# Kernel optimization log

Hardware: AMD Instinct MI355X
Metric: run time of the kernel (lower is better)

## Reference

```python
import jax, jax.numpy as jnp
import numpy as np

V, E, H, B, T, O = 100000, 300, 512, 512, 64, 2


def setup_inputs() -> dict:
    key = jax.random.key(0)
    ks = jax.random.split(key, 12)
    bound = 1.0 / np.sqrt(H)
    u = lambda k, shape: jax.random.uniform(k, shape, jnp.float32, -bound, bound)
    tokens = jax.random.randint(ks[0], (B, T), 0, V)  # int token ids
    emb = jax.random.normal(ks[1], (V, E), jnp.float32) * 0.05  # pretrained embeddings
    # GRU params stacked over 2 directions: [2, 3H, in], [2, 3H, H], [2, 3H]
    w_ih0 = u(ks[2], (2, 3 * H, E))
    w_hh0 = u(ks[3], (2, 3 * H, H))
    b_ih0 = u(ks[4], (2, 3 * H))
    b_hh0 = u(ks[5], (2, 3 * H))
    w_ih1 = u(ks[6], (2, 3 * H, 2 * H))
    w_hh1 = u(ks[7], (2, 3 * H, H))
    b_ih1 = u(ks[8], (2, 3 * H))
    b_hh1 = u(ks[9], (2, 3 * H))
    fc_w = u(ks[10], (O, 2 * H))
    fc_b = u(ks[11], (O,))
    return dict(tokens=tokens, emb=emb, w_ih0=w_ih0, w_hh0=w_hh0, b_ih0=b_ih0,
                b_hh0=b_hh0, w_ih1=w_ih1, w_hh1=w_hh1, b_ih1=b_ih1, b_hh1=b_hh1,
                fc_w=fc_w, fc_b=fc_b)


def _gru_dir(x, Wih, Whh, bih, bhh):
    # x: [B, T, in] -> [B, T, H]; PyTorch GRU cell math.
    gx = jnp.einsum('bti,gi->btg', x, Wih) + bih  # input gates precomputed [B,T,3H]
    h_units = Whh.shape[1]

    def step(h, g):
        gh = h @ Whh.T + bhh
        xr, xz, xn = jnp.split(g, 3, axis=-1)
        hr, hz, hn = jnp.split(gh, 3, axis=-1)
        r = jax.nn.sigmoid(xr + hr)
        z = jax.nn.sigmoid(xz + hz)
        n = jnp.tanh(xn + r * hn)
        h_new = (1.0 - z) * n + z * h
        return h_new, h_new

    h0 = jnp.zeros((x.shape[0], h_units), x.dtype)
    _, ys = jax.lax.scan(step, h0, jnp.swapaxes(gx, 0, 1))  # scan over time
    return jnp.swapaxes(ys, 0, 1)


def _gru_bidir(x, w_ih, w_hh, b_ih, b_hh):
    fwd = _gru_dir(x, w_ih[0], w_hh[0], b_ih[0], b_hh[0])
    bwd = _gru_dir(x[:, ::-1], w_ih[1], w_hh[1], b_ih[1], b_hh[1])[:, ::-1]
    return jnp.concatenate([fwd, bwd], axis=-1)  # [B, T, 2H]


def reference(tokens, emb, w_ih0, w_hh0, b_ih0, b_hh0, w_ih1, w_hh1, b_ih1,
              b_hh1, fc_w, fc_b):
    x = emb[tokens]                                   # [B, T, E]
    h1 = _gru_bidir(x, w_ih0, w_hh0, b_ih0, b_hh0)    # [B, T, 2H]
    h2 = _gru_bidir(h1, w_ih1, w_hh1, b_ih1, b_hh1)   # [B, T, 2H]
    # dropout output is discarded in the original forward (out = output[:, -1, :])
    last = h2[:, -1, :]                               # [B, 2H]
    return last @ fc_w.T + fc_b                       # [B, O]
```

## Files before the change

kernel.cpp:

```cpp
#include <hip/hip_runtime.h>
#include <stdint.h>


#define NTW 192
#define MTX 2048

typedef _Float16 half8 __attribute__((ext_vector_type(8)));
typedef _Float16 half4_t __attribute__((ext_vector_type(4)));
typedef float float4_t __attribute__((ext_vector_type(4)));

__device__ __forceinline__ void gl_lds16(const void* g, void* l) {
  __builtin_amdgcn_global_load_lds(
      (const __attribute__((address_space(1))) void*)g,
      (__attribute__((address_space(3))) void*)l, 16, 0, 0);
}

__device__ __forceinline__ float sigm_f(float x) { return 1.f / (1.f + __expf(-x)); }
__device__ __forceinline__ float tanh_f(float x) { return 1.f - 2.f / (__expf(2.f * x) + 1.f); }

__global__ void pack_b_kernel(const float* __restrict__ src, _Float16* __restrict__ dst,
                              int K, int KI) {
  int gid = blockIdx.x * 256 + threadIdx.x;
  int l = gid & 63, unit = gid >> 6;
  int nt = unit / KI, ks = unit - nt * KI;
  if (nt >= NTW) return;
  int row = nt * 16 + (l & 15);
  int col0 = ks * 32 + ((l >> 4) << 3);
  half8 v;
#pragma unroll
  for (int j = 0; j < 8; ++j) {
    int c = col0 + j;
    v[j] = (c < K) ? (_Float16)src[(long)row * K + c] : (_Float16)0.f;
  }
  *(half8*)(dst + (long)unit * 512 + l * 8) = v;
}

__global__ void gather_kernel(const int* __restrict__ tokens, const float* __restrict__ emb,
                              _Float16* __restrict__ x0) {
  int gid = blockIdx.x * 256 + threadIdx.x;
  int l = gid & 63, unit = gid >> 6;
  int mt = unit / 10, ks = unit - mt * 10;
  if (mt >= MTX) return;
  int row = mt * 16 + (l & 15);
  const float* e = emb + (long)tokens[row] * 300;
  int col0 = ks * 32 + ((l >> 4) << 3);
  half8 v;
#pragma unroll
  for (int j = 0; j < 8; ++j) {
    int c = col0 + j;
    v[j] = (c < 300) ? (_Float16)e[c] : (_Float16)0.f;
  }
  *(half8*)(x0 + (long)unit * 512 + l * 8) = v;
}

__global__ __launch_bounds__(256) void gemm_bt_kernel(
    const _Float16* __restrict__ A, const _Float16* __restrict__ Bw,
    const float* __restrict__ bias, _Float16* __restrict__ C, int KI) {
  __shared__ _Float16 As[8 * 512];
  __shared__ _Float16 Bs[8 * 512];
  const int bx = blockIdx.x, by = blockIdx.y;
  const int tid = threadIdx.x, w = tid >> 6, l = tid & 63;
  const int wm = w >> 1, wn = w & 1, ln = l & 15;
  const int mt0 = by * 8, nt0 = bx * 8;
  float4_t acc[4][4];
#pragma unroll
  for (int i = 0; i < 4; ++i)
#pragma unroll
    for (int j = 0; j < 4; ++j) acc[i][j] = 0.f;
  for (int it = 0; it < KI; ++it) {
    __syncthreads();
    gl_lds16(A + ((long)(mt0 + w) * KI + it) * 512 + l * 8, As + w * 512 + l * 8);
    gl_lds16(A + ((long)(mt0 + w + 4) * KI + it) * 512 + l * 8, As + (w + 4) * 512 + l * 8);
    gl_lds16(Bw + ((long)(nt0 + w) * KI + it) * 512 + l * 8, Bs + w * 512 + l * 8);
    gl_lds16(Bw + ((long)(nt0 + w + 4) * KI + it) * 512 + l * 8, Bs + (w + 4) * 512 + l * 8);
    __syncthreads();
    half8 af[4], bf[4];
#pragma unroll
    for (int i = 0; i < 4; ++i) af[i] = *(const half8*)(As + (wm * 4 + i) * 512 + l * 8);
#pragma unroll
    for (int j = 0; j < 4; ++j) bf[j] = *(const half8*)(Bs + (wn * 4 + j) * 512 + l * 8);
#pragma unroll
    for (int i = 0; i < 4; ++i)
#pragma unroll
      for (int j = 0; j < 4; ++j)
        acc[i][j] = __builtin_amdgcn_mfma_f32_16x16x32_f16(af[i], bf[j], acc[i][j], 0, 0, 0);
  }
#pragma unroll
  for (int i = 0; i < 4; ++i)
#pragma unroll
    for (int j = 0; j < 4; ++j) {
      int mt = mt0 + wm * 4 + i, ntile = nt0 + wn * 4 + j;
      float bv = bias[ntile * 16 + ln];
      half4_t o;
#pragma unroll
      for (int r = 0; r < 4; ++r) o[r] = (_Float16)(acc[i][j][r] + bv);
      *(half4_t*)(C + ((long)mt * NTW + ntile) * 256 + l * 4) = o;
    }
}

__global__ __launch_bounds__(256, 1) void gru_scan_kernel(
    const _Float16* __restrict__ whh,
    const float* __restrict__ bhh,
    const _Float16* __restrict__ gx,
    _Float16* hbuf, _Float16* ys,
    float* last,
    unsigned int* cnt) {
  __shared__ alignas(16) _Float16 hx[4 * 512];
  const int bid = blockIdx.x;
  const int d = bid >> 7, mtb = (bid >> 4) & 7, nt = bid & 15;
  const int tid = threadIdx.x, w = tid >> 6, l = tid & 63;
  const int wm = w >> 1, wn = w & 1, lq = l >> 4, ln = l & 15;
  unsigned int* flags = cnt + (d * 8 + mtb) * 16;
  const int hcol = nt * 32 + wn * 16 + ln;

  half8 bf[3][16];
#pragma unroll
  for (int g = 0; g < 3; ++g) {
    const int tg = d * 96 + g * 32 + nt * 2 + wn;
#pragma unroll
    for (int ks = 0; ks < 16; ++ks)
      bf[g][ks] = *(const half8*)(whh + (long)(tg * 16 + ks) * 512 + l * 8);
  }
  const float bh0 = bhh[d * 1536 + hcol];
  const float bh1 = bhh[d * 1536 + 512 + hcol];
  const float bh2 = bhh[d * 1536 + 1024 + hcol];
  float hreg[2][4] = {{0.f, 0.f, 0.f, 0.f}, {0.f, 0.f, 0.f, 0.f}};
  const int mtr0 = mtb * 4 + wm * 2;
  const int qh = (hcol >> 3) & 3, jh = hcol & 7;
  const int ntg0 = d * 96 + nt * 2 + wn;
  const unsigned long long* hb8 = (const unsigned long long*)hbuf;

  float xr[2][4], xz[2][4], xn[2][4];
  auto load_gx = [&](int step, float (&vr)[2][4], float (&vz)[2][4], float (&vn)[2][4]) {
    const int t2 = d ? (63 - step) : step;
    const int rm2 = t2 & 15, tq2 = t2 >> 4;
    const int eoff2 = ((rm2 >> 2) * 16 + ln) * 4 + (rm2 & 3);
#pragma unroll
    for (int i = 0; i < 2; ++i)
#pragma unroll
      for (int r = 0; r < 4; ++r) {
        const int b = (mtr0 + i) * 16 + lq * 4 + r;
        const long gbase = ((long)(b * 4 + tq2) * 192 + ntg0) * 256 + eoff2;
        vr[i][r] = (float)gx[gbase];
        vz[i][r] = (float)gx[gbase + 32 * 256];
        vn[i][r] = (float)gx[gbase + 64 * 256];
      }
  };
  load_gx(0, xr, xz, xn);

  for (int s = 0; s < 64; ++s) {
    const int par = s & 1;
    const unsigned long long* hr8 = hb8 + (long)(d * 2 + par) * 65536;
    const int t_in = d ? (63 - s) : s;
    const int rm = t_in & 15, tq = t_in >> 4;

    float4_t acc[3][2];
#pragma unroll
    for (int g = 0; g < 3; ++g) { acc[g][0] = 0.f; acc[g][1] = 0.f; }
#pragma unroll
    for (int kk = 0; kk < 2; ++kk) {
      half8 af[2][8];
#pragma unroll
      for (int i = 0; i < 2; ++i)
#pragma unroll
        for (int k2 = 0; k2 < 8; ++k2) {
          const unsigned long long* p =
              hr8 + ((long)(mtr0 + i) * 16 + kk * 8 + k2) * 128 + l * 2;
          union { half8 h; unsigned long long q[2]; } fu;
          fu.q[0] = __hip_atomic_load(p, __ATOMIC_RELAXED, __HIP_MEMORY_SCOPE_AGENT);
          fu.q[1] = __hip_atomic_load(p + 1, __ATOMIC_RELAXED, __HIP_MEMORY_SCOPE_AGENT);
          af[i][k2] = fu.h;
        }
#pragma unroll
      for (int k2 = 0; k2 < 8; ++k2)
#pragma unroll
        for (int i = 0; i < 2; ++i)
#pragma unroll
          for (int g = 0; g < 3; ++g)
            acc[g][i] = __builtin_amdgcn_mfma_f32_16x16x32_f16(af[i][k2], bf[g][kk * 8 + k2],
                                                               acc[g][i], 0, 0, 0);
    }

#pragma unroll
    for (int i = 0; i < 2; ++i) {
      const int mtile_i = mtr0 + i;
#pragma unroll
      for (int r = 0; r < 4; ++r) {
        const int b = mtile_i * 16 + lq * 4 + r;
        const long gmt = (long)b * 4 + tq;
        const float rg = sigm_f(xr[i][r] + acc[0][i][r] + bh0);
        const float zg = sigm_f(xz[i][r] + acc[1][i][r] + bh1);
        const float ng = tanh_f(xn[i][r] + rg * (acc[2][i][r] + bh2));
        const float hv = (1.f - zg) * ng + zg * hreg[i][r];
        hreg[i][r] = hv;
        hx[(wm * 2 + i) * 512 + (qh * 16 + lq * 4 + r) * 8 + jh] = (_Float16)hv;
        if (ys != nullptr) {
          const int kcol = d * 512 + hcol;
          ys[(gmt * 32 + (kcol >> 5)) * 512 + (((kcol >> 3) & 3) * 16 + rm) * 8 + (kcol & 7)] =
              (_Float16)hv;
        }
        if (last != nullptr && ((d == 0 && s == 63) || (d == 1 && s == 0)))
          last[(long)b * 1024 + d * 512 + hcol] = hv;
      }
    }
    if (s == 63) break;

    __syncthreads();
    {
      const int u = tid >> 6, lw = tid & 63;
      union { half8 h; unsigned long long q[2]; } wb;
      wb.h = *(const half8*)(hx + u * 512 + lw * 8);
      unsigned long long* dst = (unsigned long long*)hbuf +
                                (long)(d * 2 + (par ^ 1)) * 65536 +
                                ((long)((mtb * 4 + u) * 16 + nt)) * 128 + lw * 2;
      __hip_atomic_store(dst, wb.q[0], __ATOMIC_RELAXED, __HIP_MEMORY_SCOPE_AGENT);
      __hip_atomic_store(dst + 1, wb.q[1], __ATOMIC_RELAXED, __HIP_MEMORY_SCOPE_AGENT);
    }
    __syncthreads();

    if (tid == 0)
      __hip_atomic_store(flags + nt, (unsigned int)(s + 1), __ATOMIC_RELAXED,
                         __HIP_MEMORY_SCOPE_AGENT);

    load_gx(s + 1, xr, xz, xn);

    {
      const unsigned int tgt = (unsigned int)(s + 1);
      long guard = 0;
      for (;;) {
        const unsigned int f = __hip_atomic_load(flags + (l & 15), __ATOMIC_RELAXED,
                                                 __HIP_MEMORY_SCOPE_AGENT);
        if (__all((int)(f >= tgt))) break;
        __builtin_amdgcn_s_sleep(1);
        if (++guard > (1L << 24)) break;
      }
      __builtin_amdgcn_fence(__ATOMIC_ACQUIRE, "workgroup");
    }
  }
}

__global__ void fc_kernel(const float* __restrict__ lastb, const float* __restrict__ fw,
                          const float* __restrict__ fb, float* __restrict__ out) {
  const int b = blockIdx.x, l = threadIdx.x;
  const float* x = lastb + (long)b * 1024;
  float a0 = 0.f, a1 = 0.f;
  for (int k = l; k < 1024; k += 64) {
    const float v = x[k];
    a0 += v * fw[k];
    a1 += v * fw[1024 + k];
  }
#pragma unroll
  for (int off = 32; off > 0; off >>= 1) {
    a0 += __shfl_down(a0, off, 64);
    a1 += __shfl_down(a1, off, 64);
  }
  if (l == 0) {
    out[b * 2 + 0] = a0 + fb[0];
    out[b * 2 + 1] = a1 + fb[1];
  }
}

extern "C" void kernel_launch(void* const* d_in, const int* in_sizes, int n_in,
                              void* d_out, int out_size, void* d_ws, size_t ws_size,
                              hipStream_t stream) {
  const int* tokens = (const int*)d_in[0];
  const float* emb = (const float*)d_in[1];
  const float* w_ih0 = (const float*)d_in[2];
  const float* w_hh0 = (const float*)d_in[3];
  const float* b_ih0 = (const float*)d_in[4];
  const float* b_hh0 = (const float*)d_in[5];
  const float* w_ih1 = (const float*)d_in[6];
  const float* w_hh1 = (const float*)d_in[7];
  const float* b_ih1 = (const float*)d_in[8];
  const float* b_hh1 = (const float*)d_in[9];
  const float* fc_w = (const float*)d_in[10];
  const float* fc_b = (const float*)d_in[11];
  float* out = (float*)d_out;

  char* ws = (char*)d_ws;
  size_t off = 0;
  auto alloc = [&](size_t bytes) -> void* {
    void* p = ws + off;
    off += (bytes + 255) & ~(size_t)255;
    return p;
  };
  _Float16* W0f = (_Float16*)alloc(192L * 10 * 512 * 2);
  _Float16* W1f = (_Float16*)alloc(192L * 32 * 512 * 2);
  _Float16* Wh0f = (_Float16*)alloc(192L * 16 * 512 * 2);
  _Float16* Wh1f = (_Float16*)alloc(192L * 16 * 512 * 2);
  _Float16* x0f = (_Float16*)alloc(2048L * 10 * 512 * 2);
  _Float16* x1f = (_Float16*)alloc(2048L * 32 * 512 * 2);
  _Float16* gxb = (_Float16*)alloc(2048L * 192 * 256 * 2);
  char* hz = ws + off;
  _Float16* hbuf = (_Float16*)alloc(4L * 32 * 8192 * 2);
  unsigned int* cnt = (unsigned int*)alloc(4096);
  const size_t hz_bytes = 4L * 32 * 8192 * 2 + 4096;
  float* lastb = (float*)alloc(512L * 1024 * 4);
  if (off > ws_size) return;

  pack_b_kernel<<<dim3(192 * 10 * 64 / 256), 256, 0, stream>>>(w_ih0, W0f, 300, 10);
  pack_b_kernel<<<dim3(192 * 32 * 64 / 256), 256, 0, stream>>>(w_ih1, W1f, 1024, 32);
  pack_b_kernel<<<dim3(192 * 16 * 64 / 256), 256, 0, stream>>>(w_hh0, Wh0f, 512, 16);
  pack_b_kernel<<<dim3(192 * 16 * 64 / 256), 256, 0, stream>>>(w_hh1, Wh1f, 512, 16);
  gather_kernel<<<dim3(2048 * 10 * 64 / 256), 256, 0, stream>>>(tokens, emb, x0f);

  gemm_bt_kernel<<<dim3(24, 256), 256, 0, stream>>>(x0f, W0f, b_ih0, gxb, 10);
  hipMemsetAsync(hz, 0, hz_bytes, stream);
  gru_scan_kernel<<<dim3(256), 256, 0, stream>>>(Wh0f, b_hh0, gxb, hbuf, x1f, nullptr, cnt);

  gemm_bt_kernel<<<dim3(24, 256), 256, 0, stream>>>(x1f, W1f, b_ih1, gxb, 32);
  hipMemsetAsync(hz, 0, hz_bytes, stream);
  gru_scan_kernel<<<dim3(256), 256, 0, stream>>>(Wh1f, b_hh1, gxb, hbuf, nullptr, lastb, cnt);

  fc_kernel<<<dim3(512), 64, 0, stream>>>(lastb, fc_w, fc_b, out);
}
```

Before: 1.437 ms.

## Regroup scan blocks by batch rows and stage hidden state through LDS

Changes the block decomposition of the recurrent scan: each block now owns 2 M-tiles (32 batch rows) and 64 hidden columns instead of 4 M-tiles and 32 columns. Each sync group therefore shrinks from 16 to 8 blocks. Each step, the block cooperatively copies the shared hidden state once into a 32 KB LDS buffer, and all warps read it from there, replacing per-warp redundant atomic global loads. This cuts global traffic per step and lowers the barrier fan-in. The cost is an extra LDS round trip and __syncthreads per step, plus higher LDS use.

```diff
diff --git a/kernel.cpp b/kernel.cpp
--- a/kernel.cpp
+++ b/kernel.cpp
@@ -105,18 +105,19 @@
     _Float16* hbuf, _Float16* ys,
     float* last,
     unsigned int* cnt) {
+  __shared__ alignas(16) _Float16 hs[32 * 512];
   __shared__ alignas(16) _Float16 hx[4 * 512];
   const int bid = blockIdx.x;
-  const int d = bid >> 7, mtb = (bid >> 4) & 7, nt = bid & 15;
+  const int d = bid >> 7, mtg = (bid >> 3) & 15, ntb = bid & 7;
   const int tid = threadIdx.x, w = tid >> 6, l = tid & 63;
-  const int wm = w >> 1, wn = w & 1, lq = l >> 4, ln = l & 15;
-  unsigned int* flags = cnt + (d * 8 + mtb) * 16;
-  const int hcol = nt * 32 + wn * 16 + ln;
+  const int lq = l >> 4, ln = l & 15;
+  unsigned int* flags = cnt + (d * 16 + mtg) * 16;
+  const int hcol = ntb * 64 + w * 16 + ln;
 
   half8 bf[3][16];
 #pragma unroll
   for (int g = 0; g < 3; ++g) {
-    const int tg = d * 96 + g * 32 + nt * 2 + wn;
+    const int tg = d * 96 + g * 32 + ntb * 4 + w;
 #pragma unroll
     for (int ks = 0; ks < 16; ++ks)
       bf[g][ks] = *(const half8*)(whh + (long)(tg * 16 + ks) * 512 + l * 8);
@@ -125,10 +126,10 @@
   const float bh1 = bhh[d * 1536 + 512 + hcol];
   const float bh2 = bhh[d * 1536 + 1024 + hcol];
   float hreg[2][4] = {{0.f, 0.f, 0.f, 0.f}, {0.f, 0.f, 0.f, 0.f}};
-  const int mtr0 = mtb * 4 + wm * 2;
-  const int qh = (hcol >> 3) & 3, jh = hcol & 7;
-  const int ntg0 = d * 96 + nt * 2 + wn;
+  const int mtr0 = mtg * 2;
+  const int ntg0 = d * 96 + ntb * 4 + w;
   const unsigned long long* hb8 = (const unsigned long long*)hbuf;
+  unsigned long long* lds64 = (unsigned long long*)hs;
 
   float xr[2][4], xz[2][4], xn[2][4];
   auto load_gx = [&](int step, float (&vr)[2][4], float (&vz)[2][4], float (&vn)[2][4]) {
@@ -150,10 +151,33 @@
 
   for (int s = 0; s < 64; ++s) {
     const int par = s & 1;
-    const unsigned long long* hr8 = hb8 + (long)(d * 2 + par) * 65536;
     const int t_in = d ? (63 - s) : s;
     const int rm = t_in & 15, tq = t_in >> 4;
 
+    {
+      const unsigned long long* src =
+          hb8 + (long)(d * 2 + par) * 65536 + (long)mtg * 4096;
+#pragma unroll
+      for (int rr = 0; rr < 2; ++rr) {
+        unsigned long long t0[8];
+#pragma unroll
+        for (int j = 0; j < 4; ++j) {
+          const int f = (rr * 4 + j) * 256 + tid;
+          t0[j * 2] = __hip_atomic_load(src + (long)f * 2, __ATOMIC_RELAXED,
+                                        __HIP_MEMORY_SCOPE_AGENT);
+          t0[j * 2 + 1] = __hip_atomic_load(src + (long)f * 2 + 1, __ATOMIC_RELAXED,
+                                            __HIP_MEMORY_SCOPE_AGENT);
+        }
+#pragma unroll
+        for (int j = 0; j < 4; ++j) {
+          const int f = (rr * 4 + j) * 256 + tid;
+          lds64[f * 2] = t0[j * 2];
+          lds64[f * 2 + 1] = t0[j * 2 + 1];
+        }
+      }
+    }
+    __syncthreads();
+
     float4_t acc[3][2];
 #pragma unroll
     for (int g = 0; g < 3; ++g) { acc[g][0] = 0.f; acc[g][1] = 0.f; }
@@ -163,14 +187,8 @@
 #pragma unroll
       for (int i = 0; i < 2; ++i)
 #pragma unroll
-        for (int k2 = 0; k2 < 8; ++k2) {
-          const unsigned long long* p =
-              hr8 + ((long)(mtr0 + i) * 16 + kk * 8 + k2) * 128 + l * 2;
-          union { half8 h; unsigned long long q[2]; } fu;
-          fu.q[0] = __hip_atomic_load(p, __ATOMIC_RELAXED, __HIP_MEMORY_SCOPE_AGENT);
-          fu.q[1] = __hip_atomic_load(p + 1, __ATOMIC_RELAXED, __HIP_MEMORY_SCOPE_AGENT);
-          af[i][k2] = fu.h;
-        }
+        for (int k2 = 0; k2 < 8; ++k2)
+          af[i][k2] = *(const half8*)(hs + (i * 16 + kk * 8 + k2) * 512 + l * 8);
 #pragma unroll
       for (int k2 = 0; k2 < 8; ++k2)
 #pragma unroll
@@ -193,7 +211,8 @@
         const float ng = tanh_f(xn[i][r] + rg * (acc[2][i][r] + bh2));
         const float hv = (1.f - zg) * ng + zg * hreg[i][r];
         hreg[i][r] = hv;
-        hx[(wm * 2 + i) * 512 + (qh * 16 + lq * 4 + r) * 8 + jh] = (_Float16)hv;
+        hx[(i * 2 + (w >> 1)) * 512 + (((w & 1) * 2 + (ln >> 3)) * 16 + lq * 4 + r) * 8 +
+           (ln & 7)] = (_Float16)hv;
         if (ys != nullptr) {
           const int kcol = d * 512 + hcol;
           ys[(gmt * 32 + (kcol >> 5)) * 512 + (((kcol >> 3) & 3) * 16 + rm) * 8 + (kcol & 7)] =
@@ -212,14 +231,15 @@
       wb.h = *(const half8*)(hx + u * 512 + lw * 8);
       unsigned long long* dst = (unsigned long long*)hbuf +
                                 (long)(d * 2 + (par ^ 1)) * 65536 +
-                                ((long)((mtb * 4 + u) * 16 + nt)) * 128 + lw * 2;
+                                ((long)((mtg * 2 + (u >> 1)) * 16 + ntb * 2 + (u & 1))) * 128 +
+                                lw * 2;
       __hip_atomic_store(dst, wb.q[0], __ATOMIC_RELAXED, __HIP_MEMORY_SCOPE_AGENT);
       __hip_atomic_store(dst + 1, wb.q[1], __ATOMIC_RELAXED, __HIP_MEMORY_SCOPE_AGENT);
     }
     __syncthreads();
 
     if (tid == 0)
-      __hip_atomic_store(flags + nt, (unsigned int)(s + 1), __ATOMIC_RELAXED,
+      __hip_atomic_store(flags + ntb, (unsigned int)(s + 1), __ATOMIC_RELAXED,
                          __HIP_MEMORY_SCOPE_AGENT);
 
     load_gx(s + 1, xr, xz, xn);
@@ -228,7 +248,7 @@
       const unsigned int tgt = (unsigned int)(s + 1);
       long guard = 0;
       for (;;) {
-        const unsigned int f = __hip_atomic_load(flags + (l & 15), __ATOMIC_RELAXED,
+        const unsigned int f = __hip_atomic_load(flags + (l & 7), __ATOMIC_RELAXED,
                                                  __HIP_MEMORY_SCOPE_AGENT);
         if (__all((int)(f >= tgt))) break;
         __builtin_amdgcn_s_sleep(1);
```

New measurement: 1.264 ms. -12.0%, faster.

## Split GRU scan across 512 blocks with LDS-staged hidden state and streamed n-gate weights

Applied to the files above, without the earlier changes.

The persistent GRU scan now launches 512 workgroups instead of 256 (two per CU via launch bounds). Each block owns one 16-row batch tile and 64 hidden columns, and synchronises only with the 8 blocks sharing its batch tile. The hidden state is bulk-loaded into LDS once per step rather than each wave doing its own atomic global loads. To fit the register budget for two blocks per CU, only the r and z weights stay in registers and the n-gate weights are reloaded from global memory each step. The polling moves to the start of the step, so that weight reload overlaps the wait. This trades more per-step weight traffic and more blocks to coordinate for higher occupancy and a smaller working set per block.

```diff
diff --git a/kernel.cpp b/kernel.cpp
--- a/kernel.cpp
+++ b/kernel.cpp
@@ -98,144 +98,163 @@
     }
 }
 
-__global__ __launch_bounds__(256, 1) void gru_scan_kernel(
+__global__ __launch_bounds__(256, 2) void gru_scan_kernel(
     const _Float16* __restrict__ whh,
     const float* __restrict__ bhh,
     const _Float16* __restrict__ gx,
     _Float16* hbuf, _Float16* ys,
     float* last,
     unsigned int* cnt) {
-  __shared__ alignas(16) _Float16 hx[4 * 512];
+  __shared__ alignas(16) _Float16 hs[16 * 512];
+  __shared__ alignas(16) _Float16 hx[2 * 512];
   const int bid = blockIdx.x;
-  const int d = bid >> 7, mtb = (bid >> 4) & 7, nt = bid & 15;
+  const int d = bid >> 8, rt = (bid >> 3) & 31, ntb = bid & 7;
   const int tid = threadIdx.x, w = tid >> 6, l = tid & 63;
-  const int wm = w >> 1, wn = w & 1, lq = l >> 4, ln = l & 15;
-  unsigned int* flags = cnt + (d * 8 + mtb) * 16;
-  const int hcol = nt * 32 + wn * 16 + ln;
-
-  half8 bf[3][16];
-#pragma unroll
-  for (int g = 0; g < 3; ++g) {
-    const int tg = d * 96 + g * 32 + nt * 2 + wn;
-#pragma unroll
-    for (int ks = 0; ks < 16; ++ks)
-      bf[g][ks] = *(const half8*)(whh + (long)(tg * 16 + ks) * 512 + l * 8);
+  const int lq = l >> 4, ln = l & 15;
+  unsigned int* flags = cnt + (d * 32 + rt) * 16;
+  const int hcol = ntb * 64 + w * 16 + ln;
+
+  const int tgr = d * 96 + ntb * 4 + w;
+  const int tgz = tgr + 32;
+  const int tgn = tgr + 64;
+  half8 bfr[16], bfz[16];
+#pragma unroll
+  for (int ks = 0; ks < 16; ++ks) {
+    bfr[ks] = *(const half8*)(whh + (long)(tgr * 16 + ks) * 512 + l * 8);
+    bfz[ks] = *(const half8*)(whh + (long)(tgz * 16 + ks) * 512 + l * 8);
   }
   const float bh0 = bhh[d * 1536 + hcol];
   const float bh1 = bhh[d * 1536 + 512 + hcol];
   const float bh2 = bhh[d * 1536 + 1024 + hcol];
-  float hreg[2][4] = {{0.f, 0.f, 0.f, 0.f}, {0.f, 0.f, 0.f, 0.f}};
-  const int mtr0 = mtb * 4 + wm * 2;
-  const int qh = (hcol >> 3) & 3, jh = hcol & 7;
-  const int ntg0 = d * 96 + nt * 2 + wn;
+  float hreg[4] = {0.f, 0.f, 0.f, 0.f};
+  const int ntg0 = d * 96 + ntb * 4 + w;
   const unsigned long long* hb8 = (const unsigned long long*)hbuf;
-
-  float xr[2][4], xz[2][4], xn[2][4];
-  auto load_gx = [&](int step, float (&vr)[2][4], float (&vz)[2][4], float (&vn)[2][4]) {
+  unsigned long long* hb8w = (unsigned long long*)hbuf;
+  unsigned long long* lds64 = (unsigned long long*)hs;
+  const unsigned long long* hx64 = (const unsigned long long*)hx;
+
+  float xr[4], xz[4], xn[4];
+  auto load_gx = [&](int step) {
     const int t2 = d ? (63 - step) : step;
     const int rm2 = t2 & 15, tq2 = t2 >> 4;
     const int eoff2 = ((rm2 >> 2) * 16 + ln) * 4 + (rm2 & 3);
 #pragma unroll
-    for (int i = 0; i < 2; ++i)
-#pragma unroll
-      for (int r = 0; r < 4; ++r) {
-        const int b = (mtr0 + i) * 16 + lq * 4 + r;
-        const long gbase = ((long)(b * 4 + tq2) * 192 + ntg0) * 256 + eoff2;
-        vr[i][r] = (float)gx[gbase];
-        vz[i][r] = (float)gx[gbase + 32 * 256];
-        vn[i][r] = (float)gx[gbase + 64 * 256];
-      }
+    for (int r = 0; r < 4; ++r) {
+      const int b = rt * 16 + lq * 4 + r;
+      const long gbase = ((long)(b * 4 + tq2) * 192 + ntg0) * 256 + eoff2;
+      xr[r] = (float)gx[gbase];
+      xz[r] = (float)gx[gbase + 32 * 256];
+      xn[r] = (float)gx[gbase + 64 * 256];
+    }
   };
-  load_gx(0, xr, xz, xn);
+  load_gx(0);
+
+  auto poll = [&](unsigned int tgt) {
+    long guard = 0;
+    for (;;) {
+      const unsigned int f = __hip_atomic_load(flags + (l & 7), __ATOMIC_RELAXED,
+                                               __HIP_MEMORY_SCOPE_AGENT);
+      if (__all((int)(f >= tgt))) break;
+      __builtin_amdgcn_s_sleep(1);
+      if (++guard > (1L << 24)) break;
+    }
+  };
 
   for (int s = 0; s < 64; ++s) {
     const int par = s & 1;
-    const unsigned long long* hr8 = hb8 + (long)(d * 2 + par) * 65536;
     const int t_in = d ? (63 - s) : s;
     const int rm = t_in & 15, tq = t_in >> 4;
-
-    float4_t acc[3][2];
-#pragma unroll
-    for (int g = 0; g < 3; ++g) { acc[g][0] = 0.f; acc[g][1] = 0.f; }
-#pragma unroll
-    for (int kk = 0; kk < 2; ++kk) {
-      half8 af[2][8];
-#pragma unroll
-      for (int i = 0; i < 2; ++i)
-#pragma unroll
-        for (int k2 = 0; k2 < 8; ++k2) {
-          const unsigned long long* p =
-              hr8 + ((long)(mtr0 + i) * 16 + kk * 8 + k2) * 128 + l * 2;
-          union { half8 h; unsigned long long q[2]; } fu;
-          fu.q[0] = __hip_atomic_load(p, __ATOMIC_RELAXED, __HIP_MEMORY_SCOPE_AGENT);
-          fu.q[1] = __hip_atomic_load(p + 1, __ATOMIC_RELAXED, __HIP_MEMORY_SCOPE_AGENT);
-          af[i][k2] = fu.h;
-        }
-#pragma unroll
-      for (int k2 = 0; k2 < 8; ++k2)
-#pragma unroll
-        for (int i = 0; i < 2; ++i)
-#pragma unroll
-          for (int g = 0; g < 3; ++g)
-            acc[g][i] = __builtin_amdgcn_mfma_f32_16x16x32_f16(af[i][k2], bf[g][kk * 8 + k2],
-                                                               acc[g][i], 0, 0, 0);
-    }
-
-#pragma unroll
-    for (int i = 0; i < 2; ++i) {
-      const int mtile_i = mtr0 + i;
-#pragma unroll
-      for (int r = 0; r < 4; ++r) {
-        const int b = mtile_i * 16 + lq * 4 + r;
-        const long gmt = (long)b * 4 + tq;
-        const float rg = sigm_f(xr[i][r] + acc[0][i][r] + bh0);
-        const float zg = sigm_f(xz[i][r] + acc[1][i][r] + bh1);
-        const float ng = tanh_f(xn[i][r] + rg * (acc[2][i][r] + bh2));
-        const float hv = (1.f - zg) * ng + zg * hreg[i][r];
-        hreg[i][r] = hv;
-        hx[(wm * 2 + i) * 512 + (qh * 16 + lq * 4 + r) * 8 + jh] = (_Float16)hv;
-        if (ys != nullptr) {
-          const int kcol = d * 512 + hcol;
-          ys[(gmt * 32 + (kcol >> 5)) * 512 + (((kcol >> 3) & 3) * 16 + rm) * 8 + (kcol & 7)] =
-              (_Float16)hv;
-        }
-        if (last != nullptr && ((d == 0 && s == 63) || (d == 1 && s == 0)))
-          last[(long)b * 1024 + d * 512 + hcol] = hv;
+    const unsigned long long* src =
+        hb8 + (long)(d * 2 + par) * 65536 + (long)rt * 2048;
+
+    half8 bn0[8];
+#pragma unroll
+    for (int k = 0; k < 8; ++k)
+      bn0[k] = *(const half8*)(whh + (long)(tgn * 16 + k) * 512 + l * 8);
+
+    poll((unsigned int)s);
+    __builtin_amdgcn_fence(__ATOMIC_ACQUIRE, "workgroup");
+
+    unsigned long long ta[8];
+#pragma unroll
+    for (int j = 0; j < 8; ++j)
+      ta[j] = __hip_atomic_load(src + j * 256 + tid, __ATOMIC_RELAXED,
+                                __HIP_MEMORY_SCOPE_AGENT);
+#pragma unroll
+    for (int j = 0; j < 8; ++j) lds64[j * 256 + tid] = ta[j];
+    __syncthreads();
+
+    half8 bn1[8];
+#pragma unroll
+    for (int k = 0; k < 8; ++k)
+      bn1[k] = *(const half8*)(whh + (long)(tgn * 16 + 8 + k) * 512 + l * 8);
+
+    float4_t accr, accz, accn;
+    accr = 0.f; accz = 0.f; accn = 0.f;
+#pragma unroll
+    for (int c = 0; c < 2; ++c) {
+      half8 af[4];
+#pragma unroll
+      for (int k = 0; k < 4; ++k)
+        af[k] = *(const half8*)(hs + (c * 4 + k) * 512 + l * 8);
+#pragma unroll
+      for (int k = 0; k < 4; ++k) {
+        const int ks = c * 4 + k;
+        accr = __builtin_amdgcn_mfma_f32_16x16x32_f16(af[k], bfr[ks], accr, 0, 0, 0);
+        accz = __builtin_amdgcn_mfma_f32_16x16x32_f16(af[k], bfz[ks], accz, 0, 0, 0);
+        accn = __builtin_amdgcn_mfma_f32_16x16x32_f16(af[k], bn0[ks], accn, 0, 0, 0);
       }
     }
+#pragma unroll
+    for (int c = 0; c < 2; ++c) {
+      half8 af[4];
+#pragma unroll
+      for (int k = 0; k < 4; ++k)
+        af[k] = *(const half8*)(hs + ((8 + c * 4 + k)) * 512 + l * 8);
+#pragma unroll
+      for (int k = 0; k < 4; ++k) {
+        const int ks = 8 + c * 4 + k;
+        accr = __builtin_amdgcn_mfma_f32_16x16x32_f16(af[k], bfr[ks], accr, 0, 0, 0);
+        accz = __builtin_amdgcn_mfma_f32_16x16x32_f16(af[k], bfz[ks], accz, 0, 0, 0);
+        accn = __builtin_amdgcn_mfma_f32_16x16x32_f16(af[k], bn1[c * 4 + k], accn, 0, 0, 0);
+      }
+    }
+
+#pragma unroll
+    for (int r = 0; r < 4; ++r) {
+      const int b = rt * 16 + lq * 4 + r;
+      const long gmt = (long)b * 4 + tq;
+      const float rg = sigm_f(xr[r] + accr[r] + bh0);
+      const float zg = sigm_f(xz[r] + accz[r] + bh1);
+      const float ng = tanh_f(xn[r] + rg * (accn[r] + bh2));
+      const float hv = (1.f - zg) * ng + zg * hreg[r];
+      hreg[r] = hv;
+      hx[(w >> 1) * 512 + (((w & 1) * 2 + (ln >> 3)) * 16 + lq * 4 + r) * 8 + (ln & 7)] =
+          (_Float16)hv;
+      if (ys != nullptr) {
+        const int kcol = d * 512 + hcol;
+        ys[(gmt * 32 + (kcol >> 5)) * 512 + (((kcol >> 3) & 3) * 16 + rm) * 8 + (kcol & 7)] =
+            (_Float16)hv;
+      }
+      if (last != nullptr && ((d == 0 && s == 63) || (d == 1 && s == 0)))
+        last[(long)b * 1024 + d * 512 + hcol] = hv;
+    }
     if (s == 63) break;
 
     __syncthreads();
     {
-      const int u = tid >> 6, lw = tid & 63;
-      union { half8 h; unsigned long long q[2]; } wb;
-      wb.h = *(const half8*)(hx + u * 512 + lw * 8);
-      unsigned long long* dst = (unsigned long long*)hbuf +
-                                (long)(d * 2 + (par ^ 1)) * 65536 +
-                                ((long)((mtb * 4 + u) * 16 + nt)) * 128 + lw * 2;
-      __hip_atomic_store(dst, wb.q[0], __ATOMIC_RELAXED, __HIP_MEMORY_SCOPE_AGENT);
-      __hip_atomic_store(dst + 1, wb.q[1], __ATOMIC_RELAXED, __HIP_MEMORY_SCOPE_AGENT);
+      const unsigned long long q = hx64[tid];
+      unsigned long long* dst = hb8w + (long)(d * 2 + (par ^ 1)) * 65536 +
+                                ((long)rt * 16 + ntb * 2 + (tid >> 7)) * 128 + (tid & 127);
+      __hip_atomic_store(dst, q, __ATOMIC_RELAXED, __HIP_MEMORY_SCOPE_AGENT);
     }
     __syncthreads();
 
     if (tid == 0)
-      __hip_atomic_store(flags + nt, (unsigned int)(s + 1), __ATOMIC_RELAXED,
+      __hip_atomic_store(flags + ntb, (unsigned int)(s + 1), __ATOMIC_RELAXED,
                          __HIP_MEMORY_SCOPE_AGENT);
 
-    load_gx(s + 1, xr, xz, xn);
-
-    {
-      const unsigned int tgt = (unsigned int)(s + 1);
-      long guard = 0;
-      for (;;) {
-        const unsigned int f = __hip_atomic_load(flags + (l & 15), __ATOMIC_RELAXED,
-                                                 __HIP_MEMORY_SCOPE_AGENT);
-        if (__all((int)(f >= tgt))) break;
-        __builtin_amdgcn_s_sleep(1);
-        if (++guard > (1L << 24)) break;
-      }
-      __builtin_amdgcn_fence(__ATOMIC_ACQUIRE, "workgroup");
-    }
+    load_gx(s + 1);
   }
 }
 
@@ -306,11 +325,11 @@
 
   gemm_bt_kernel<<<dim3(24, 256), 256, 0, stream>>>(x0f, W0f, b_ih0, gxb, 10);
   hipMemsetAsync(hz, 0, hz_bytes, stream);
-  gru_scan_kernel<<<dim3(256), 256, 0, stream>>>(Wh0f, b_hh0, gxb, hbuf, x1f, nullptr, cnt);
+  gru_scan_kernel<<<dim3(512), 256, 0, stream>>>(Wh0f, b_hh0, gxb, hbuf, x1f, nullptr, cnt);
 
   gemm_bt_kernel<<<dim3(24, 256), 256, 0, stream>>>(x1f, W1f, b_ih1, gxb, 32);
   hipMemsetAsync(hz, 0, hz_bytes, stream);
-  gru_scan_kernel<<<dim3(256), 256, 0, stream>>>(Wh1f, b_hh1, gxb, hbuf, nullptr, lastb, cnt);
+  gru_scan_kernel<<<dim3(512), 256, 0, stream>>>(Wh1f, b_hh1, gxb, hbuf, nullptr, lastb, cnt);
 
   fc_kernel<<<dim3(512), 64, 0, stream>>>(lastb, fc_w, fc_b, out);
 }
```

Result: faster. 1.258 ms (-12.5%).
